# Performance work log

Hardware: AMD Instinct MI355X
Metric: run time of the kernel (lower is better)

## Reference

```python
import jax, jax.numpy as jnp
import numpy as np

B, N, ND, ED = 4, 24, 13, 12          # batch, num_nodes, node feat dim, edge feat dim
H, NH, HD = 256, 8, 32                # hidden, heads, head dim (H == NH*HD)
L, T = 64, 1000                       # transformer layers, max_timestep
_SCALE = 1.0 / float(np.sqrt(H))      # torch divides by sqrt(node_dim)=sqrt(256)


def _ln(x, g, b):
    m = x.mean(-1, keepdims=True)
    v = ((x - m) ** 2).mean(-1, keepdims=True)
    return (x - m) / jnp.sqrt(v + 1e-5) * g + b


def setup_inputs() -> dict:
    key = jax.random.key(0)
    it = iter(jax.random.split(key, 40))
    def w(*s):
        return (jax.random.normal(next(it), s) * 0.02).astype(jnp.float32)
    z = lambda *s: jnp.zeros(s, jnp.float32)
    o = lambda *s: jnp.ones(s, jnp.float32)
    d = {}
    d['nodes'] = jax.random.normal(next(it), (B, N, ND), jnp.float32)
    d['edges'] = jax.random.normal(next(it), (B, N, N, ED), jnp.float32)
    d['conds'] = jax.random.randint(next(it), (B,), 0, T)
    # input MLPs
    d['inN_w1'] = w(ND, H); d['inN_b1'] = z(H); d['inN_w2'] = w(H, H); d['inN_b2'] = z(H)
    d['inE_w1'] = w(ED, H); d['inE_b1'] = z(H); d['inE_w2'] = w(H, H); d['inE_b2'] = z(H)
    d['inC_w1'] = w(T, H);  d['inC_b1'] = z(H); d['inC_w2'] = w(H, H); d['inC_b2'] = z(H)
    # stacked per-layer params (leading dim L, scanned)
    d['qkv_w'] = w(L, H, 3 * H); d['qkv_b'] = z(L, 3 * H)
    d['no_w'] = w(L, H, H); d['no_b'] = z(L, H)
    d['eo_w'] = w(L, H, H); d['eo_b'] = z(L, H)
    d['ln1n_g'] = o(L, H); d['ln1n_b'] = z(L, H)
    d['ln1e_g'] = o(L, H); d['ln1e_b'] = z(L, H)
    d['mn_w1'] = w(L, H, 4 * H); d['mn_b1'] = z(L, 4 * H)
    d['mn_w2'] = w(L, 4 * H, H); d['mn_b2'] = z(L, H)
    d['me_w1'] = w(L, H, 4 * H); d['me_b1'] = z(L, 4 * H)
    d['me_w2'] = w(L, 4 * H, H); d['me_b2'] = z(L, H)
    d['ln2n_g'] = o(L, H); d['ln2n_b'] = z(L, H)
    d['ln2e_g'] = o(L, H); d['ln2e_b'] = z(L, H)
    # output MLPs
    d['outN_w1'] = w(H, H); d['outN_b1'] = z(H); d['outN_w2'] = w(H, ND); d['outN_b2'] = z(ND)
    d['outE_w1'] = w(H, H); d['outE_b1'] = z(H); d['outE_w2'] = w(H, ED); d['outE_b2'] = z(ED)
    return d


def _forward(nodes, edges, conds,
             inN_w1, inN_b1, inN_w2, inN_b2, inE_w1, inE_b1, inE_w2, inE_b2,
             inC_w1, inC_b1, inC_w2, inC_b2,
             qkv_w, qkv_b, no_w, no_b, eo_w, eo_b,
             ln1n_g, ln1n_b, ln1e_g, ln1e_b,
             mn_w1, mn_b1, mn_w2, mn_b2, me_w1, me_b1, me_w2, me_b2,
             ln2n_g, ln2n_b, ln2e_g, ln2e_b,
             outN_w1, outN_b1, outN_w2, outN_b2, outE_w1, outE_b1, outE_w2, outE_b2):
    relu = jax.nn.relu
    c = jax.nn.one_hot(conds, T, dtype=nodes.dtype)
    c = relu(relu(c @ inC_w1 + inC_b1) @ inC_w2 + inC_b2)          # (B,H)
    n = relu(relu(nodes @ inN_w1 + inN_b1) @ inN_w2 + inN_b2)      # (B,N,H)
    e = relu(relu(edges @ inE_w1 + inE_b1) @ inE_w2 + inE_b2)      # (B,N,N,H)

    def layer(carry, p):
        n, e = carry
        (qw, qb, nw, nb, ew, eb, g1n, b1n, g1e, b1e,
         w1n, bb1n, w2n, bb2n, w1e, bb1e, w2e, bb2e, g2n, b2n, g2e, b2e) = p
        nc = n + c[:, None, :]
        q, k, v = jnp.split(nc @ qw + qb, 3, axis=-1)
        q = q.reshape(B, N, NH, HD); k = k.reshape(B, N, NH, HD); v = v.reshape(B, N, NH, HD)
        s5 = jnp.einsum('bihd,bjhd->bijhd', q, k) * _SCALE          # (B,N,N,NH,HD)
        ne5 = s5 + e.reshape(B, N, N, NH, HD)                       # edge-biased scores
        attn = jax.nn.softmax(ne5.sum(-1), axis=2)                  # (B,N,N,NH)
        wv = jnp.einsum('bijh,bjhd->bihd', attn, v).reshape(B, N, H)
        an = _ln(wv @ nw + nb + n, g1n, b1n)
        ae = _ln(relu(ne5.reshape(B, N, N, H) @ ew + eb) + e, g1e, b1e)
        n2 = _ln(relu(an @ w1n + bb1n) @ w2n + bb2n + an, g2n, b2n)
        e2 = _ln(relu(ae @ w1e + bb1e) @ w2e + bb2e + ae, g2e, b2e)
        return (n2, e2), None

    stacked = (qkv_w, qkv_b, no_w, no_b, eo_w, eo_b, ln1n_g, ln1n_b, ln1e_g, ln1e_b,
               mn_w1, mn_b1, mn_w2, mn_b2, me_w1, me_b1, me_w2, me_b2,
               ln2n_g, ln2n_b, ln2e_g, ln2e_b)
    (n, e), _ = jax.lax.scan(layer, (n, e), stacked)
    out_n = relu(n @ outN_w1 + outN_b1) @ outN_w2 + outN_b2
    out_e = relu(e @ outE_w1 + outE_b1) @ outE_w2 + outE_b2
    return out_n, out_e


def reference(nodes, edges, conds,
              inN_w1, inN_b1, inN_w2, inN_b2, inE_w1, inE_b1, inE_w2, inE_b2,
              inC_w1, inC_b1, inC_w2, inC_b2,
              qkv_w, qkv_b, no_w, no_b, eo_w, eo_b,
              ln1n_g, ln1n_b, ln1e_g, ln1e_b,
              mn_w1, mn_b1, mn_w2, mn_b2, me_w1, me_b1, me_w2, me_b2,
              ln2n_g, ln2n_b, ln2e_g, ln2e_b,
              outN_w1, outN_b1, outN_w2, outN_b2, outE_w1, outE_b1, outE_w2, outE_b2):
    return _forward(nodes, edges, conds,
                    inN_w1, inN_b1, inN_w2, inN_b2, inE_w1, inE_b1, inE_w2, inE_b2,
                    inC_w1, inC_b1, inC_w2, inC_b2,
                    qkv_w, qkv_b, no_w, no_b, eo_w, eo_b,
                    ln1n_g, ln1n_b, ln1e_g, ln1e_b,
                    mn_w1, mn_b1, mn_w2, mn_b2, me_w1, me_b1, me_w2, me_b2,
                    ln2n_g, ln2n_b, ln2e_g, ln2e_b,
                    outN_w1, outN_b1, outN_w2, outN_b2, outE_w1, outE_b1, outE_w2, outE_b2)
```

## Files before the change

kernel.cpp:

```cpp
#include <hip/hip_runtime.h>

typedef _Float16 half_t;
typedef _Float16 f16x8 __attribute__((ext_vector_type(8)));
typedef _Float16 f16x4 __attribute__((ext_vector_type(4)));
typedef float f32x4 __attribute__((ext_vector_type(4)));

#define BB 4
#define NNODE 24
#define NLAYER 64
#define SCALE_QK 0.0625f

#define WS_C     0
#define WS_N     1024
#define WS_NACC  25600
#define NACC_STRIDE 24576
#define WS_E     74752
#define WS_AE32  664576
#define WS_AE16  1254400
#define WS_AN16  1549312
#define WS_EPART 1561600
#define EPART_SLICE 589824
#define WS_WTF   3920896
#define SLOT_F16 1376256
#define OFF_QKVT 0
#define OFF_NOT  196608
#define OFF_EOT  262144
#define OFF_MN1T 327680
#define OFF_MN2T 589824
#define OFF_ME1T 851968
#define OFF_ME2T 1114112
#define OFF_INE2T  (3*SLOT_F16)
#define OFF_OUTE1T (3*SLOT_F16 + 65536)

struct Params {
  const float *nodes, *edges; const int* conds;
  const float *inN_w1,*inN_b1,*inN_w2,*inN_b2;
  const float *inE_w1,*inE_b1,*inE_w2,*inE_b2;
  const float *inC_w1,*inC_b1,*inC_w2,*inC_b2;
  const float *qkv_w,*qkv_b,*no_w,*no_b,*eo_w,*eo_b;
  const float *ln1n_g,*ln1n_b,*ln1e_g,*ln1e_b;
  const float *mn_w1,*mn_b1,*mn_w2,*mn_b2,*me_w1,*me_b1,*me_w2,*me_b2;
  const float *ln2n_g,*ln2n_b,*ln2e_g,*ln2e_b;
  const float *outN_w1,*outN_b1,*outN_w2,*outN_b2,*outE_w1,*outE_b1,*outE_w2,*outE_b2;
  float* ws; float* out;
};

template<int NT, int KS, int MT, int LDAH>
__device__ __forceinline__ void gemm_rs_acc(const half_t* __restrict__ WT, int ldb,
                                            const char* __restrict__ A,
                                            f32x4 (&acc)[NT][MT]) {
  const int lane = threadIdx.x & 63;
  const int wv = threadIdx.x >> 6;
  const int l15 = lane & 15;
  const int kg = lane >> 4;
  f16x8 b[NT][KS];
#pragma unroll
  for (int nt = 0; nt < NT; ++nt) {
    const int col = (nt * 8 + wv) * 16 + l15;
#pragma unroll
    for (int ks = 0; ks < KS; ++ks)
      b[nt][ks] = *(const f16x8*)(WT + (size_t)col * ldb + ks * 32 + kg * 8);
  }
#pragma unroll
  for (int m = 0; m < MT; ++m) {
    f16x8 a[KS];
    const int row = m * 16 + l15;
#pragma unroll
    for (int ks = 0; ks < KS; ++ks)
      a[ks] = *(const f16x8*)(A + row * (LDAH * 2) + (((ks * 32 + kg * 8) * 2) ^ ((row & 7) << 4)));
#pragma unroll
    for (int ks = 0; ks < KS; ++ks)
#pragma unroll
      for (int nt = 0; nt < NT; ++nt)
        acc[nt][m] = __builtin_amdgcn_mfma_f32_16x16x32_f16(a[ks], b[nt][ks], acc[nt][m], 0, 0, 0);
  }
}

template<int NT, int KS, int MT, int LDAH, typename EPI>
__device__ __forceinline__ void gemm_rs(const half_t* __restrict__ WT, int ldb,
                                        const char* __restrict__ A, EPI epi) {
  f32x4 acc[NT][MT];
#pragma unroll
  for (int nt = 0; nt < NT; ++nt)
#pragma unroll
    for (int m = 0; m < MT; ++m) {
      f32x4 z = {0.f, 0.f, 0.f, 0.f};
      acc[nt][m] = z;
    }
  gemm_rs_acc<NT, KS, MT, LDAH>(WT, ldb, A, acc);
#pragma unroll
  for (int nt = 0; nt < NT; ++nt)
#pragma unroll
    for (int m = 0; m < MT; ++m)
      epi(nt, m, acc[nt][m]);
}

template<int NTW, int KT, int MT, int LDA, int LDB, typename EPI>
__device__ __forceinline__ void run_gemm_s(const half_t* __restrict__ WT,
                                           const char* __restrict__ A,
                                           EPI epi) {
  const int lane = threadIdx.x & 63;
  const int wv = threadIdx.x >> 6;
  const int l15 = lane & 15;
  const int kg = lane >> 4;
  constexpr int NC = KT / 8;
  constexpr int TC = NC * NTW;
  f16x8 bb[2][8];
  auto ldb = [&](int c, int w) {
    const int kc = c / NTW, n = c % NTW;
    const half_t* bp = WT + (size_t)((n * 8 + wv) * 16 + l15) * LDB + kc * 256 + kg * 8;
#pragma unroll
    for (int q = 0; q < 8; ++q) bb[w][q] = *(const f16x8*)(bp + q * 32);
  };
  f32x4 acc[NTW][MT];
#pragma unroll
  for (int n = 0; n < NTW; ++n)
#pragma unroll
    for (int m = 0; m < MT; ++m) {
      f32x4 z = {0.f, 0.f, 0.f, 0.f};
      acc[n][m] = z;
    }
  ldb(0, 0);
#pragma unroll
  for (int kc = 0; kc < NC; ++kc) {
    f16x8 a[8][MT];
#pragma unroll
    for (int q = 0; q < 8; ++q) {
      const int k0 = (kc * 8 + q) * 32 + kg * 8;
#pragma unroll
      for (int m = 0; m < MT; ++m) {
        const int row = m * 16 + l15;
        a[q][m] = *(const f16x8*)(A + row * (LDA * 2) + ((k0 * 2) ^ ((row & 7) << 4)));
      }
    }
#pragma unroll
    for (int n = 0; n < NTW; ++n) {
      const int c = kc * NTW + n;
      if (c + 1 < TC) ldb(c + 1, (c + 1) & 1);
#pragma unroll
      for (int q = 0; q < 8; ++q)
#pragma unroll
        for (int m = 0; m < MT; ++m)
          acc[n][m] = __builtin_amdgcn_mfma_f32_16x16x32_f16(a[q][m], bb[c & 1][q], acc[n][m], 0, 0, 0);
    }
  }
#pragma unroll
  for (int n = 0; n < NTW; ++n) epi(n, acc[n]);
}

__device__ void conv_matrix_tile(const float* __restrict__ src, half_t* __restrict__ dst,
                                 int K, int Nn, int tk, int tn, char* smem) {
  float* tl = (float*)smem;
  const int t = threadIdx.x;
  const int c = t & 63;
  const int r0 = t >> 6;
  for (int r = r0; r < 64; r += 8)
    tl[r * 65 + c] = src[(size_t)(tk * 64 + r) * Nn + tn * 64 + c];
  __syncthreads();
  for (int r = r0; r < 64; r += 8)
    dst[(size_t)(tn * 64 + r) * K + tk * 64 + c] = (half_t)tl[c * 65 + r];
  __syncthreads();
}

__device__ void conv_layer_tile(const Params& p, half_t* slot, int lw, int tile, char* smem) {
  if (tile < 48)       { conv_matrix_tile(p.qkv_w + (size_t)lw*196608, slot+OFF_QKVT, 256, 768, tile & 3, tile >> 2, smem); }
  else if (tile < 64)  { int t2 = tile-48;  conv_matrix_tile(p.no_w  + (size_t)lw*65536,  slot+OFF_NOT,  256, 256, t2 & 3,  t2 >> 2, smem); }
  else if (tile < 80)  { int t2 = tile-64;  conv_matrix_tile(p.eo_w  + (size_t)lw*65536,  slot+OFF_EOT,  256, 256, t2 & 3,  t2 >> 2, smem); }
  else if (tile < 144) { int t2 = tile-80;  conv_matrix_tile(p.mn_w1 + (size_t)lw*262144, slot+OFF_MN1T, 256, 1024, t2 & 3, t2 >> 2, smem); }
  else if (tile < 208) { int t2 = tile-144; conv_matrix_tile(p.mn_w2 + (size_t)lw*262144, slot+OFF_MN2T, 1024, 256, t2 & 15, t2 >> 4, smem); }
  else if (tile < 272) { int t2 = tile-208; conv_matrix_tile(p.me_w1 + (size_t)lw*262144, slot+OFF_ME1T, 256, 1024, t2 & 3, t2 >> 2, smem); }
  else                 { int t2 = tile-272; conv_matrix_tile(p.me_w2 + (size_t)lw*262144, slot+OFF_ME2T, 1024, 256, t2 & 15, t2 >> 4, smem); }
}

__global__ __launch_bounds__(512, 2) void k_embedA(Params p) {
  __shared__ __align__(16) char smem[17024];
  const int bid = blockIdx.x, tid = threadIdx.x;
  float* ws = p.ws;
  half_t* wt = (half_t*)(ws + WS_WTF);
  if (bid < 4) {
    const int b = bid;
    const int cond = p.conds[b];
    float* t1 = (float*)smem;
    if (tid < 256) t1[tid] = fmaxf(p.inC_w1[(size_t)cond * 256 + tid] + p.inC_b1[tid], 0.f);
    __syncthreads();
    if (tid < 256) {
      float s = p.inC_b2[tid];
      for (int k = 0; k < 256; ++k) s += t1[k] * p.inC_w2[(size_t)k * 256 + tid];
      ws[WS_C + b * 256 + tid] = fmaxf(s, 0.f);
    }
  } else {
    for (int job = bid - 4; job < 704; job += 128) {
      if (job < 336)      conv_layer_tile(p, wt, 0, job, smem);
      else if (job < 672) conv_layer_tile(p, wt + SLOT_F16, 1, job - 336, smem);
      else if (job < 688) { int t2 = job - 672; conv_matrix_tile(p.inE_w2,  wt + OFF_INE2T,  256, 256, t2 & 3, t2 >> 2, smem); }
      else                { int t2 = job - 688; conv_matrix_tile(p.outE_w1, wt + OFF_OUTE1T, 256, 256, t2 & 3, t2 >> 2, smem); }
    }
  }
}

__global__ __launch_bounds__(512, 2) void k_embedB(Params p) {
  __shared__ __align__(16) char smem[24640];
  const int bid = blockIdx.x, tid = threadIdx.x;
  const int lane = tid & 63, wv = tid >> 6, l15 = lane & 15, kg = lane >> 4;
  float* ws = p.ws;
  half_t* wt = (half_t*)(ws + WS_WTF);
  float* e0 = ws + WS_E;
  float* n0 = ws + WS_N;
  if (bid < 96) {
    const int b = bid / NNODE, i = bid % NNODE;
    float* eb = (float*)smem;
    char* t16 = smem + 2048;
    for (int idx = tid; idx < 24 * 12; idx += 512)
      eb[idx] = p.edges[((size_t)(b * NNODE + i) * NNODE + idx / 12) * 12 + idx % 12];
    __syncthreads();
    for (int idx = tid; idx < 32 * 32; idx += 512) {
      int r = idx >> 5, kb = idx & 31, k0 = kb * 8;
      f16x8 v;
#pragma unroll
      for (int j = 0; j < 8; ++j) v[j] = (half_t)0.f;
      if (r < NNODE) {
#pragma unroll
        for (int j = 0; j < 8; ++j) {
          int col = k0 + j;
          float s = p.inE_b1[col];
          for (int kk = 0; kk < 12; ++kk) s += eb[r * 12 + kk] * p.inE_w1[kk * 256 + col];
          v[j] = (half_t)fmaxf(s, 0.f);
        }
      }
      *(f16x8*)(t16 + r * 512 + ((k0 * 2) ^ ((r & 7) << 4))) = v;
    }
    __syncthreads();
    run_gemm_s<2, 8, 2, 256, 256>(wt + OFF_INE2T, t16,
      [&](int n, f32x4 (&accn)[2]) {
        const int col = (n * 8 + wv) * 16 + l15;
        const float bcol = p.inE_b2[col];
#pragma unroll
        for (int m = 0; m < 2; ++m)
#pragma unroll
          for (int r4 = 0; r4 < 4; ++r4) {
            const int row = m * 16 + kg * 4 + r4;
            if (row < NNODE)
              e0[((size_t)(b * NNODE + i) * NNODE + row) * 256 + col] = fmaxf(accn[m][r4] + bcol, 0.f);
          }
      });
  } else {
    const int nb = bid - 96, b = nb >> 1, hf = nb & 1, i0 = hf * 12;
    float* nd = (float*)smem;
    float* t1 = (float*)(smem + 1024);
    for (int idx = tid; idx < 12 * 13; idx += 512)
      nd[(idx / 13) * 16 + (idx % 13)] = p.nodes[(size_t)(b * NNODE + i0 + idx / 13) * 13 + idx % 13];
    __syncthreads();
    for (int idx = tid; idx < 12 * 256; idx += 512) {
      int r = idx >> 8, col = idx & 255;
      float s = p.inN_b1[col];
      for (int kk = 0; kk < 13; ++kk) s += nd[r * 16 + kk] * p.inN_w1[kk * 256 + col];
      t1[r * 257 + col] = fmaxf(s, 0.f);
    }
    __syncthreads();
    {
      int col = tid & 255, rh = tid >> 8;
      float a6[6] = {0.f, 0.f, 0.f, 0.f, 0.f, 0.f};
      for (int k = 0; k < 256; ++k) {
        float w = p.inN_w2[(size_t)k * 256 + col];
#pragma unroll
        for (int r = 0; r < 6; ++r) a6[r] += t1[(rh * 6 + r) * 257 + k] * w;
      }
#pragma unroll
      for (int r = 0; r < 6; ++r) {
        int row = rh * 6 + r;
        n0[(size_t)(b * NNODE + i0 + row) * 256 + col] = fmaxf(a6[r] + p.inN_b2[col], 0.f);
      }
    }
  }
}

__global__ __launch_bounds__(512, 2) void k_attn(Params p, int lyr) {
  __shared__ __align__(16) char smem[139488];
  const int bid = blockIdx.x, tid = threadIdx.x;
  const int lane = tid & 63, wv = tid >> 6, l15 = lane & 15, kg = lane >> 4;
  float* ws = p.ws;
  half_t* wt = (half_t*)(ws + WS_WTF);
  const half_t* slot = wt + (size_t)(lyr % 3) * SLOT_F16;

  if (bid >= 96) {
    if (lyr + 2 < NLAYER) {
      half_t* dslot = wt + (size_t)((lyr + 2) % 3) * SLOT_F16;
      for (int tile = bid - 96; tile < 336; tile += 126)
        conv_layer_tile(p, dslot, lyr + 2, tile, smem);
    }
    return;
  }
  const int b = bid / NNODE, i = bid % NNODE;
  const size_t rowbase = (size_t)(b * NNODE + i) * NNODE;
  char* nc16 = smem;
  half_t* qkv16 = (half_t*)(smem + 16384);
  char* ne5 = smem + 65536;
  float* e32 = (float*)(smem + 81920);
  float* psum = (float*)(smem + 106880);
  float* sc = (float*)(smem + 109952);
  float* wvl = (float*)(smem + 110720);
  float* ni = (float*)(smem + 111744);
  float* anr = (float*)(smem + 112768);
  float* aef = (float*)(smem + 114816);
  float* ae32 = ws + WS_AE32;
  half_t* ae16g = (half_t*)(ws + WS_AE16);
  const half_t* epart = (const half_t*)(ws + WS_EPART);
  const float* nacc_in = ws + WS_NACC + ((lyr + 1) & 1) * NACC_STRIDE;
  float* nacc_out = ws + WS_NACC + (lyr & 1) * NACC_STRIDE;
  const float* cb = ws + WS_C + b * 256;

  for (int r = wv; r < 32; r += 8) {
    const int c = lane * 4;
    f16x4 hv;
    if (r < NNODE) {
      f32x4 y;
      if (lyr == 0) {
        y = *(const f32x4*)(ws + WS_N + (size_t)(b * NNODE + r) * 256 + c);
      } else {
        f32x4 x = *(const f32x4*)(nacc_in + (size_t)(b * NNODE + r) * 256 + c);
        float s = x[0] + x[1] + x[2] + x[3];
        float s2 = x[0]*x[0] + x[1]*x[1] + x[2]*x[2] + x[3]*x[3];
#pragma unroll
        for (int off = 32; off; off >>= 1) { s += __shfl_xor(s, off); s2 += __shfl_xor(s2, off); }
        float mean = s * (1.f / 256.f);
        float rstd = rsqrtf(s2 * (1.f / 256.f) - mean * mean + 1e-5f);
        const float* g = p.ln2n_g + (size_t)(lyr - 1) * 256;
        const float* bv = p.ln2n_b + (size_t)(lyr - 1) * 256;
#pragma unroll
        for (int j = 0; j < 4; ++j) y[j] = (x[j] - mean) * rstd * g[c + j] + bv[c + j];
      }
      if (r == i) *(f32x4*)(ni + c) = y;
#pragma unroll
      for (int j = 0; j < 4; ++j) hv[j] = (half_t)(y[j] + cb[c + j]);
    } else {
#pragma unroll
      for (int j = 0; j < 4; ++j) hv[j] = (half_t)0.f;
    }
    *(f16x4*)(nc16 + r * 512 + ((lane * 8) ^ ((r & 7) << 4))) = hv;
  }
  __syncthreads();
  {
    const float* qb = p.qkv_b + (size_t)lyr * 768;
#pragma unroll
    for (int nn = 0; nn < 3; ++nn) {
      gemm_rs<2, 8, 2, 256>(slot + OFF_QKVT + (size_t)(nn * 256) * 256, 256, nc16,
        [&](int nt, int m, f32x4 v) {
          const int gcol = nn * 256 + (nt * 8 + wv) * 16 + l15;
          const float bc = qb[gcol];
#pragma unroll
          for (int r4 = 0; r4 < 4; ++r4) {
            const int row = m * 16 + kg * 4 + r4;
            qkv16[(size_t)row * 768 + gcol] = (half_t)(v[r4] + bc);
          }
        });
    }
  }
  __syncthreads();
  for (int idx = tid; idx < 32 * 32; idx += 512) {
    int r = idx >> 5, kb = idx & 31, k0 = kb * 8;
    f16x8 v;
#pragma unroll
    for (int j = 0; j < 8; ++j) v[j] = (half_t)0.f;
    if (r < NNODE) {
      const size_t row = rowbase + r;
      float x[8];
      if (lyr == 0) {
        const f32x4 a = *(const f32x4*)(ws + WS_E + row * 256 + k0);
        const f32x4 b4 = *(const f32x4*)(ws + WS_E + row * 256 + k0 + 4);
#pragma unroll
        for (int j = 0; j < 4; ++j) { x[j] = a[j]; x[4 + j] = b4[j]; }
      } else {
        const float* mb2 = p.me_b2 + (size_t)(lyr - 1) * 256;
        const f32x4 a = *(const f32x4*)(ae32 + row * 256 + k0);
        const f32x4 b4 = *(const f32x4*)(ae32 + row * 256 + k0 + 4);
#pragma unroll
        for (int j = 0; j < 4; ++j) { x[j] = a[j] + mb2[k0 + j]; x[4 + j] = b4[j] + mb2[k0 + 4 + j]; }
#pragma unroll
        for (int hb = 0; hb < 8; ++hb) {
          f16x8 pv = *(const f16x8*)(epart + (size_t)hb * EPART_SLICE + row * 256 + k0);
#pragma unroll
          for (int j = 0; j < 8; ++j) x[j] += (float)pv[j];
        }
        float s = 0.f, s2 = 0.f;
#pragma unroll
        for (int j = 0; j < 8; ++j) { s += x[j]; s2 += x[j] * x[j]; }
#pragma unroll
        for (int off = 16; off; off >>= 1) { s += __shfl_xor(s, off); s2 += __shfl_xor(s2, off); }
        float mean = s * (1.f / 256.f);
        float rstd = rsqrtf(s2 * (1.f / 256.f) - mean * mean + 1e-5f);
        const float* g = p.ln2e_g + (size_t)(lyr - 1) * 256;
        const float* bv = p.ln2e_b + (size_t)(lyr - 1) * 256;
#pragma unroll
        for (int j = 0; j < 8; ++j) x[j] = (x[j] - mean) * rstd * g[k0 + j] + bv[k0 + j];
      }
      f16x8 q8 = *(const f16x8*)(qkv16 + (size_t)i * 768 + k0);
      f16x8 k8 = *(const f16x8*)(qkv16 + (size_t)r * 768 + 256 + k0);
      float ps = 0.f;
#pragma unroll
      for (int j = 0; j < 8; ++j) {
        float f = SCALE_QK * (float)q8[j] * (float)k8[j] + x[j];
        v[j] = (half_t)f;
        ps += f;
        e32[r * 260 + k0 + j] = x[j];
      }
      psum[r * 32 + kb] = ps;
    }
    *(f16x8*)(ne5 + r * 512 + ((k0 * 2) ^ ((r & 7) << 4))) = v;
  }
  __syncthreads();
  if (tid < 192) {
    int hq = tid & 7;
    sc[tid] = psum[(tid >> 3) * 32 + hq * 4] + psum[(tid >> 3) * 32 + hq * 4 + 1] +
              psum[(tid >> 3) * 32 + hq * 4 + 2] + psum[(tid >> 3) * 32 + hq * 4 + 3];
  }
  __syncthreads();
  if (tid < 8) {
    const int h = tid;
    float mx = -1e30f;
#pragma unroll
    for (int j = 0; j < 24; ++j) mx = fmaxf(mx, sc[j * 8 + h]);
    float ex[24]; float ssum = 0.f;
#pragma unroll
    for (int j = 0; j < 24; ++j) { ex[j] = __expf(sc[j * 8 + h] - mx); ssum += ex[j]; }
    float inv = 1.f / ssum;
#pragma unroll
    for (int j = 0; j < 24; ++j) sc[j * 8 + h] = ex[j] * inv;
  }
  __syncthreads();
  if (tid < 256) {
    const int d = tid, h = d >> 5;
    float a = 0.f;
#pragma unroll
    for (int j = 0; j < 24; ++j) a += sc[j * 8 + h] * (float)qkv16[(size_t)j * 768 + 512 + d];
    wvl[d] = a;
  }
  {
    const float* eob = p.eo_b + (size_t)lyr * 256;
    gemm_rs<2, 8, 2, 256>(slot + OFF_EOT, 256, ne5,
      [&](int nt, int m, f32x4 v) {
        const int col = (nt * 8 + wv) * 16 + l15;
#pragma unroll
        for (int r4 = 0; r4 < 4; ++r4) {
          const int row = m * 16 + kg * 4 + r4;
          if (row < NNODE)
            aef[row * 257 + col] = fmaxf(v[r4] + eob[col], 0.f) + e32[row * 260 + col];
        }
      });
  }
  __syncthreads();
  {
    const float* g = p.ln1e_g + (size_t)lyr * 256;
    const float* bv = p.ln1e_b + (size_t)lyr * 256;
    for (int r = wv; r < NNODE; r += 8) {
      float x[4];
#pragma unroll
      for (int j = 0; j < 4; ++j) x[j] = aef[r * 257 + lane * 4 + j];
      float s = x[0] + x[1] + x[2] + x[3];
      float s2 = x[0]*x[0] + x[1]*x[1] + x[2]*x[2] + x[3]*x[3];
#pragma unroll
      for (int off = 32; off; off >>= 1) { s += __shfl_xor(s, off); s2 += __shfl_xor(s2, off); }
      float mean = s * (1.f / 256.f);
      float rstd = rsqrtf(s2 * (1.f / 256.f) - mean * mean + 1e-5f);
      f16x4 hv; f32x4 yv;
#pragma unroll
      for (int j = 0; j < 4; ++j) {
        int c = lane * 4 + j;
        float y = (x[j] - mean) * rstd * g[c] + bv[c];
        yv[j] = y; hv[j] = (half_t)y;
      }
      *(f32x4*)(ae32 + (rowbase + r) * 256 + lane * 4) = yv;
      *(f16x4*)(ae16g + (rowbase + r) * 256 + lane * 4) = hv;
    }
  }
  {
    const half_t* NOT_ = slot + OFF_NOT;
    int c = tid & 255, hf = tid >> 8;
    float s = 0.f;
    const half_t* wp = NOT_ + (size_t)c * 256 + hf * 128;
#pragma unroll
    for (int k8 = 0; k8 < 16; ++k8) {
      f16x8 w8 = *(const f16x8*)(wp + k8 * 8);
#pragma unroll
      for (int j = 0; j < 8; ++j) s += wvl[hf * 128 + k8 * 8 + j] * (float)w8[j];
    }
    anr[hf * 256 + c] = s;
  }
  __syncthreads();
  if (wv == 0) {
    const float* nob = p.no_b + (size_t)lyr * 256;
    const float* g = p.ln1n_g + (size_t)lyr * 256;
    const float* bv = p.ln1n_b + (size_t)lyr * 256;
    const float* mb2 = p.mn_b2 + (size_t)lyr * 256;
    float x[4];
#pragma unroll
    for (int j = 0; j < 4; ++j) {
      int c = lane * 4 + j;
      x[j] = anr[c] + anr[256 + c] + nob[c] + ni[c];
    }
    float s = x[0] + x[1] + x[2] + x[3];
    float s2 = x[0]*x[0] + x[1]*x[1] + x[2]*x[2] + x[3]*x[3];
#pragma unroll
    for (int off = 32; off; off >>= 1) { s += __shfl_xor(s, off); s2 += __shfl_xor(s2, off); }
    float mean = s * (1.f / 256.f);
    float rstd = rsqrtf(s2 * (1.f / 256.f) - mean * mean + 1e-5f);
    f16x4 hv; f32x4 av;
#pragma unroll
    for (int j = 0; j < 4; ++j) {
      int c = lane * 4 + j;
      float y = (x[j] - mean) * rstd * g[c] + bv[c];
      hv[j] = (half_t)y;
      av[j] = y + mb2[c];
    }
    *(f16x4*)((half_t*)(ws + WS_AN16) + (size_t)(b * NNODE + i) * 256 + lane * 4) = hv;
    *(f32x4*)(nacc_out + (size_t)(b * NNODE + i) * 256 + lane * 4) = av;
  }
}

__global__ __launch_bounds__(512, 2) void k_mlp(Params p, int lyr) {
  __shared__ __align__(16) char smem[73728];
  const int bid = blockIdx.x, tid = threadIdx.x;
  const int lane = tid & 63, wv = tid >> 6, l15 = lane & 15, kg = lane >> 4;
  float* ws = p.ws;
  half_t* wt = (half_t*)(ws + WS_WTF);
  const half_t* slot = wt + (size_t)(lyr % 3) * SLOT_F16;

  if (bid < 192) {
    const int rb = bid >> 3, hb = bid & 7;
    const int row0 = rb * 96;
    char* A16 = smem;
    char* hl = smem + 49152;
    const half_t* aeg = (const half_t*)(ws + WS_AE16) + (size_t)row0 * 256;
    for (int idx = tid; idx < 96 * 32; idx += 512) {
      int r = idx >> 5, c8 = idx & 31;
      f16x8 v = *(const f16x8*)(aeg + r * 256 + c8 * 8);
      *(f16x8*)(A16 + r * 512 + ((c8 * 16) ^ ((r & 7) << 4))) = v;
    }
    __syncthreads();
    const float* mb1 = p.me_b1 + (size_t)lyr * 1024 + hb * 128;
    gemm_rs<1, 8, 6, 256>(slot + OFF_ME1T + (size_t)(hb * 128) * 256, 256, A16,
      [&](int nt, int m, f32x4 v) {
        const int colb = wv * 16 + l15;
        const float bc = mb1[colb];
#pragma unroll
        for (int r4 = 0; r4 < 4; ++r4) {
          const int row = m * 16 + kg * 4 + r4;
          *(half_t*)(hl + row * 256 + ((colb * 2) ^ ((row & 7) << 4))) = (half_t)fmaxf(v[r4] + bc, 0.f);
        }
      });
    __syncthreads();
    half_t* ep = (half_t*)(ws + WS_EPART) + (size_t)hb * EPART_SLICE + (size_t)row0 * 256;
    gemm_rs<2, 4, 6, 128>(slot + OFF_ME2T + hb * 128, 1024, hl,
      [&](int nt, int m, f32x4 v) {
        const int col = (nt * 8 + wv) * 16 + l15;
#pragma unroll
        for (int r4 = 0; r4 < 4; ++r4)
          ep[(size_t)(m * 16 + kg * 4 + r4) * 256 + col] = (half_t)v[r4];
      });
  } else {
    const int hb = bid - 192;
    char* A16 = smem;
    char* hl = smem + 49152;
    const half_t* ang = (const half_t*)(ws + WS_AN16);
    for (int idx = tid; idx < 96 * 32; idx += 512) {
      int r = idx >> 5, c8 = idx & 31;
      f16x8 v = *(const f16x8*)(ang + (size_t)r * 256 + c8 * 8);
      *(f16x8*)(A16 + r * 512 + ((c8 * 16) ^ ((r & 7) << 4))) = v;
    }
    __syncthreads();
    const float* mb1 = p.mn_b1 + (size_t)lyr * 1024 + hb * 128;
    gemm_rs<1, 8, 6, 256>(slot + OFF_MN1T + (size_t)(hb * 128) * 256, 256, A16,
      [&](int nt, int m, f32x4 v) {
        const int colb = wv * 16 + l15;
        const float bc = mb1[colb];
#pragma unroll
        for (int r4 = 0; r4 < 4; ++r4) {
          const int row = m * 16 + kg * 4 + r4;
          *(half_t*)(hl + row * 256 + ((colb * 2) ^ ((row & 7) << 4))) = (half_t)fmaxf(v[r4] + bc, 0.f);
        }
      });
    __syncthreads();
    float* nacc_out = ws + WS_NACC + (lyr & 1) * NACC_STRIDE;
    gemm_rs<2, 4, 6, 128>(slot + OFF_MN2T + hb * 128, 1024, hl,
      [&](int nt, int m, f32x4 v) {
        const int col = (nt * 8 + wv) * 16 + l15;
#pragma unroll
        for (int r4 = 0; r4 < 4; ++r4)
          atomicAdd(&nacc_out[(size_t)(m * 16 + kg * 4 + r4) * 256 + col], v[r4]);
      });
  }
}

__global__ __launch_bounds__(512, 2) void k_out(Params p) {
  __shared__ __align__(16) char smem[49472];
  const int bid = blockIdx.x, tid = threadIdx.x;
  const int lane = tid & 63, wv = tid >> 6, l15 = lane & 15, kg = lane >> 4;
  float* ws = p.ws;
  half_t* wt = (half_t*)(ws + WS_WTF);
  const float* ae32 = ws + WS_AE32;
  const half_t* epart = (const half_t*)(ws + WS_EPART);
  if (bid < 96) {
    const int b = bid / NNODE, i = bid % NNODE;
    const size_t rowbase = (size_t)(b * NNODE + i) * NNODE;
    char* A16 = smem;
    float* h2f = (float*)(smem + 16384);
    const float* mb2 = p.me_b2 + (size_t)63 * 256;
    const float* g = p.ln2e_g + (size_t)63 * 256;
    const float* bvv = p.ln2e_b + (size_t)63 * 256;
    for (int idx = tid; idx < 32 * 32; idx += 512) {
      int r = idx >> 5, kb = idx & 31, k0 = kb * 8;
      f16x8 v;
#pragma unroll
      for (int j = 0; j < 8; ++j) v[j] = (half_t)0.f;
      if (r < NNODE) {
        const size_t row = rowbase + r;
        float x[8];
        const f32x4 a = *(const f32x4*)(ae32 + row * 256 + k0);
        const f32x4 b4 = *(const f32x4*)(ae32 + row * 256 + k0 + 4);
#pragma unroll
        for (int j = 0; j < 4; ++j) { x[j] = a[j] + mb2[k0 + j]; x[4 + j] = b4[j] + mb2[k0 + 4 + j]; }
#pragma unroll
        for (int hb = 0; hb < 8; ++hb) {
          f16x8 pv = *(const f16x8*)(epart + (size_t)hb * EPART_SLICE + row * 256 + k0);
#pragma unroll
          for (int j = 0; j < 8; ++j) x[j] += (float)pv[j];
        }
        float s = 0.f, s2 = 0.f;
#pragma unroll
        for (int j = 0; j < 8; ++j) { s += x[j]; s2 += x[j] * x[j]; }
#pragma unroll
        for (int off = 16; off; off >>= 1) { s += __shfl_xor(s, off); s2 += __shfl_xor(s2, off); }
        float mean = s * (1.f / 256.f);
        float rstd = rsqrtf(s2 * (1.f / 256.f) - mean * mean + 1e-5f);
#pragma unroll
        for (int j = 0; j < 8; ++j)
          v[j] = (half_t)((x[j] - mean) * rstd * g[k0 + j] + bvv[k0 + j]);
      }
      *(f16x8*)(A16 + r * 512 + ((k0 * 2) ^ ((r & 7) << 4))) = v;
    }
    __syncthreads();
    run_gemm_s<2, 8, 2, 256, 256>(wt + OFF_OUTE1T, A16,
      [&](int n, f32x4 (&accn)[2]) {
        const int col = (n * 8 + wv) * 16 + l15;
#pragma unroll
        for (int m = 0; m < 2; ++m)
#pragma unroll
          for (int r4 = 0; r4 < 4; ++r4) {
            const int row = m * 16 + kg * 4 + r4;
            h2f[row * 257 + col] = (row < NNODE) ? fmaxf(accn[m][r4] + p.outE_b1[col], 0.f) : 0.f;
          }
      });
    __syncthreads();
    for (int pr = tid; pr < 24 * 12; pr += 512) {
      int j = pr / 12, oc = pr % 12;
      float s = p.outE_b2[oc];
      for (int k = 0; k < 256; ++k) s += h2f[j * 257 + k] * p.outE_w2[k * 12 + oc];
      p.out[1248 + ((size_t)(b * NNODE + i) * NNODE + j) * 12 + oc] = s;
    }
  } else {
    const int nb = bid - 96, bq = nb >> 1, hf = nb & 1, i0 = hf * 12;
    float* nl = (float*)smem;
    float* t1f = (float*)(smem + 12544);
    const float* n_acc = ws + WS_NACC + 1 * NACC_STRIDE;
    const float* g = p.ln2n_g + (size_t)63 * 256;
    const float* bvv = p.ln2n_b + (size_t)63 * 256;
    for (int r = wv; r < 12; r += 8) {
      const int row = bq * NNODE + i0 + r;
      const int c = lane * 4;
      f32x4 x = *(const f32x4*)(n_acc + (size_t)row * 256 + c);
      float s = x[0] + x[1] + x[2] + x[3];
      float s2 = x[0]*x[0] + x[1]*x[1] + x[2]*x[2] + x[3]*x[3];
#pragma unroll
      for (int off = 32; off; off >>= 1) { s += __shfl_xor(s, off); s2 += __shfl_xor(s2, off); }
      float mean = s * (1.f / 256.f);
      float rstd = rsqrtf(s2 * (1.f / 256.f) - mean * mean + 1e-5f);
      f32x4 y;
#pragma unroll
      for (int j = 0; j < 4; ++j) y[j] = (x[j] - mean) * rstd * g[c + j] + bvv[c + j];
      *(f32x4*)(nl + r * 257 + c) = y;
    }
    __syncthreads();
    {
      int col = tid & 255, rh = tid >> 8;
      float a6[6] = {0.f, 0.f, 0.f, 0.f, 0.f, 0.f};
      for (int k = 0; k < 256; ++k) {
        float w = p.outN_w1[(size_t)k * 256 + col];
#pragma unroll
        for (int r = 0; r < 6; ++r) a6[r] += nl[(rh * 6 + r) * 257 + k] * w;
      }
#pragma unroll
      for (int r = 0; r < 6; ++r)
        t1f[(rh * 6 + r) * 257 + col] = fmaxf(a6[r] + p.outN_b1[col], 0.f);
    }
    __syncthreads();
    for (int pr = tid; pr < 12 * 13; pr += 512) {
      int il = pr / 13, oc = pr % 13;
      float s = p.outN_b2[oc];
      for (int k = 0; k < 256; ++k) s += t1f[il * 257 + k] * p.outN_w2[k * 13 + oc];
      p.out[((size_t)(bq * NNODE) + i0 + il) * 13 + oc] = s;
    }
  }
}

extern "C" void kernel_launch(void* const* d_in, const int* in_sizes, int n_in,
                              void* d_out, int out_size, void* d_ws, size_t ws_size,
                              hipStream_t stream) {
  (void)in_sizes; (void)n_in; (void)out_size; (void)ws_size;
  Params p;
  const float* const* fi = (const float* const*)d_in;
  p.nodes = fi[0]; p.edges = fi[1]; p.conds = (const int*)d_in[2];
  p.inN_w1 = fi[3]; p.inN_b1 = fi[4]; p.inN_w2 = fi[5]; p.inN_b2 = fi[6];
  p.inE_w1 = fi[7]; p.inE_b1 = fi[8]; p.inE_w2 = fi[9]; p.inE_b2 = fi[10];
  p.inC_w1 = fi[11]; p.inC_b1 = fi[12]; p.inC_w2 = fi[13]; p.inC_b2 = fi[14];
  p.qkv_w = fi[15]; p.qkv_b = fi[16]; p.no_w = fi[17]; p.no_b = fi[18];
  p.eo_w = fi[19]; p.eo_b = fi[20];
  p.ln1n_g = fi[21]; p.ln1n_b = fi[22]; p.ln1e_g = fi[23]; p.ln1e_b = fi[24];
  p.mn_w1 = fi[25]; p.mn_b1 = fi[26]; p.mn_w2 = fi[27]; p.mn_b2 = fi[28];
  p.me_w1 = fi[29]; p.me_b1 = fi[30]; p.me_w2 = fi[31]; p.me_b2 = fi[32];
  p.ln2n_g = fi[33]; p.ln2n_b = fi[34]; p.ln2e_g = fi[35]; p.ln2e_b = fi[36];
  p.outN_w1 = fi[37]; p.outN_b1 = fi[38]; p.outN_w2 = fi[39]; p.outN_b2 = fi[40];
  p.outE_w1 = fi[41]; p.outE_b1 = fi[42]; p.outE_w2 = fi[43]; p.outE_b2 = fi[44];
  p.ws = (float*)d_ws; p.out = (float*)d_out;

  k_embedA<<<dim3(132), dim3(512), 0, stream>>>(p);
  k_embedB<<<dim3(104), dim3(512), 0, stream>>>(p);
  for (int l = 0; l < NLAYER; ++l) {
    k_attn<<<dim3(222), dim3(512), 0, stream>>>(p, l);
    k_mlp<<<dim3(200), dim3(512), 0, stream>>>(p, l);
  }
  k_out<<<dim3(104), dim3(512), 0, stream>>>(p);
}
```

Baseline: 2.953 ms.

## Prefetch MLP weights before staging, merge QKV passes, parallelize softmax

In the MLP kernel, the first-GEMM weight fragments are loaded into registers before the activation tile is staged into shared memory, so the global weight latency overlaps the staging and the barrier. The QKV projection now runs as two passes of three N-tiles instead of three passes of two. The per-head softmax moves from 8 serial threads to 256 threads using wave shuffles for the max and sum. Holding the prefetched weights raises register pressure under the 512x2 launch bounds.

```diff
diff --git a/kernel.cpp b/kernel.cpp
--- a/kernel.cpp
+++ b/kernel.cpp
@@ -95,6 +95,37 @@
       epi(nt, m, acc[nt][m]);
 }
 
+template<int KS>
+__device__ __forceinline__ void load_b1(const half_t* __restrict__ WT, int ldb, f16x8 (&b)[KS]) {
+  const int lane = threadIdx.x & 63, wvq = threadIdx.x >> 6;
+  const int col = wvq * 16 + (lane & 15), kg = lane >> 4;
+#pragma unroll
+  for (int ks = 0; ks < KS; ++ks)
+    b[ks] = *(const f16x8*)(WT + (size_t)col * ldb + ks * 32 + kg * 8);
+}
+
+template<int KS, int MT, int LDAH, typename EPI>
+__device__ __forceinline__ void gemm_rs_preb(const f16x8 (&b)[KS], const char* __restrict__ A, EPI epi) {
+  const int lane = threadIdx.x & 63;
+  const int l15 = lane & 15, kg = lane >> 4;
+  f32x4 acc[MT];
+#pragma unroll
+  for (int m = 0; m < MT; ++m) { f32x4 z = {0.f,0.f,0.f,0.f}; acc[m] = z; }
+#pragma unroll
+  for (int m = 0; m < MT; ++m) {
+    const int row = m * 16 + l15;
+    f16x8 a[KS];
+#pragma unroll
+    for (int ks = 0; ks < KS; ++ks)
+      a[ks] = *(const f16x8*)(A + row * (LDAH * 2) + (((ks * 32 + kg * 8) * 2) ^ ((row & 7) << 4)));
+#pragma unroll
+    for (int ks = 0; ks < KS; ++ks)
+      acc[m] = __builtin_amdgcn_mfma_f32_16x16x32_f16(a[ks], b[ks], acc[m], 0, 0, 0);
+  }
+#pragma unroll
+  for (int m = 0; m < MT; ++m) epi(m, acc[m]);
+}
+
 template<int NTW, int KT, int MT, int LDA, int LDB, typename EPI>
 __device__ __forceinline__ void run_gemm_s(const half_t* __restrict__ WT,
                                            const char* __restrict__ A,
@@ -342,10 +373,10 @@
   {
     const float* qb = p.qkv_b + (size_t)lyr * 768;
 #pragma unroll
-    for (int nn = 0; nn < 3; ++nn) {
-      gemm_rs<2, 8, 2, 256>(slot + OFF_QKVT + (size_t)(nn * 256) * 256, 256, nc16,
+    for (int h2 = 0; h2 < 2; ++h2) {
+      gemm_rs<3, 8, 2, 256>(slot + OFF_QKVT + (size_t)(h2 * 384) * 256, 256, nc16,
         [&](int nt, int m, f32x4 v) {
-          const int gcol = nn * 256 + (nt * 8 + wv) * 16 + l15;
+          const int gcol = h2 * 384 + (nt * 8 + wv) * 16 + l15;
           const float bc = qb[gcol];
 #pragma unroll
           for (int r4 = 0; r4 < 4; ++r4) {
@@ -414,17 +445,17 @@
               psum[(tid >> 3) * 32 + hq * 4 + 2] + psum[(tid >> 3) * 32 + hq * 4 + 3];
   }
   __syncthreads();
-  if (tid < 8) {
-    const int h = tid;
-    float mx = -1e30f;
-#pragma unroll
-    for (int j = 0; j < 24; ++j) mx = fmaxf(mx, sc[j * 8 + h]);
-    float ex[24]; float ssum = 0.f;
-#pragma unroll
-    for (int j = 0; j < 24; ++j) { ex[j] = __expf(sc[j * 8 + h] - mx); ssum += ex[j]; }
-    float inv = 1.f / ssum;
-#pragma unroll
-    for (int j = 0; j < 24; ++j) sc[j * 8 + h] = ex[j] * inv;
+  if (tid < 256) {
+    const int h = tid >> 5, j = tid & 31;
+    float v = (j < 24) ? sc[j * 8 + h] : -1e30f;
+    float mx = v;
+#pragma unroll
+    for (int off = 16; off; off >>= 1) mx = fmaxf(mx, __shfl_xor(mx, off));
+    float ex = (j < 24) ? __expf(v - mx) : 0.f;
+    float sum = ex;
+#pragma unroll
+    for (int off = 16; off; off >>= 1) sum += __shfl_xor(sum, off);
+    if (j < 24) sc[j * 8 + h] = ex / sum;
   }
   __syncthreads();
   if (tid < 256) {
@@ -529,6 +560,8 @@
     const int row0 = rb * 96;
     char* A16 = smem;
     char* hl = smem + 49152;
+    f16x8 b1[8];
+    load_b1<8>(slot + OFF_ME1T + (size_t)(hb * 128) * 256, 256, b1);
     const half_t* aeg = (const half_t*)(ws + WS_AE16) + (size_t)row0 * 256;
     for (int idx = tid; idx < 96 * 32; idx += 512) {
       int r = idx >> 5, c8 = idx & 31;
@@ -537,8 +570,8 @@
     }
     __syncthreads();
     const float* mb1 = p.me_b1 + (size_t)lyr * 1024 + hb * 128;
-    gemm_rs<1, 8, 6, 256>(slot + OFF_ME1T + (size_t)(hb * 128) * 256, 256, A16,
-      [&](int nt, int m, f32x4 v) {
+    gemm_rs_preb<8, 6, 256>(b1, A16,
+      [&](int m, f32x4 v) {
         const int colb = wv * 16 + l15;
         const float bc = mb1[colb];
 #pragma unroll
@@ -560,6 +593,8 @@
     const int hb = bid - 192;
     char* A16 = smem;
     char* hl = smem + 49152;
+    f16x8 b1[8];
+    load_b1<8>(slot + OFF_MN1T + (size_t)(hb * 128) * 256, 256, b1);
     const half_t* ang = (const half_t*)(ws + WS_AN16);
     for (int idx = tid; idx < 96 * 32; idx += 512) {
       int r = idx >> 5, c8 = idx & 31;
@@ -568,8 +603,8 @@
     }
     __syncthreads();
     const float* mb1 = p.mn_b1 + (size_t)lyr * 1024 + hb * 128;
-    gemm_rs<1, 8, 6, 256>(slot + OFF_MN1T + (size_t)(hb * 128) * 256, 256, A16,
-      [&](int nt, int m, f32x4 v) {
+    gemm_rs_preb<8, 6, 256>(b1, A16,
+      [&](int m, f32x4 v) {
         const int colb = wv * 16 + l15;
         const float bc = mb1[colb];
 #pragma unroll
```

After: 3.014 ms. 1.02x slower.
